# Performance work log

Measured on AMD Instinct MI355X. Metric: run time of the kernel, lower is better.

## Reference

```python
import jax, jax.numpy as jnp
import numpy as np

SEQ_LEN, BATCH, INPUT_SIZE, HIDDEN = 512, 64, 256, 512


def setup_inputs() -> dict:
    key = jax.random.key(0)
    k_x, k_wih, k_whh, k_bih, k_bhh = jax.random.split(key, 5)
    bound = 1.0 / np.sqrt(HIDDEN)  # torch nn.RNN init: U(-1/sqrt(H), 1/sqrt(H))
    x = jax.random.normal(k_x, (SEQ_LEN, BATCH, INPUT_SIZE), dtype=jnp.float32)
    h0 = jnp.zeros((1, BATCH, HIDDEN), dtype=jnp.float32)
    W_ih = jax.random.uniform(k_wih, (HIDDEN, INPUT_SIZE), minval=-bound, maxval=bound, dtype=jnp.float32)
    W_hh = jax.random.uniform(k_whh, (HIDDEN, HIDDEN), minval=-bound, maxval=bound, dtype=jnp.float32)
    b_ih = jax.random.uniform(k_bih, (HIDDEN,), minval=-bound, maxval=bound, dtype=jnp.float32)
    b_hh = jax.random.uniform(k_bhh, (HIDDEN,), minval=-bound, maxval=bound, dtype=jnp.float32)
    return {"x": x, "h0": h0, "W_ih": W_ih, "W_hh": W_hh, "b_ih": b_ih, "b_hh": b_hh}


def reference(x, h0, W_ih, W_hh, b_ih, b_hh):
    # Elman RNN: h_t = tanh(W_ih x_t + b_ih + W_hh h_{t-1} + b_hh)
    # Precompute the input projection for all timesteps (one big GEMM),
    # then scan the sequential recurrence.
    xW = jnp.einsum('tbi,hi->tbh', x, W_ih) + b_ih + b_hh  # (T, B, H)

    def step(h, xw_t):
        h_new = jnp.tanh(xw_t + h @ W_hh.T)  # (B, H)
        return h_new, h_new

    h_last, h_seq = jax.lax.scan(step, h0[0], xW)
    return h_seq, h_last[None]  # (T, B, H), (1, B, H)
```

## Files before the change

### kernel.cpp

```cpp
#include <hip/hip_runtime.h>


#define T_LEN 512
#define NBATCH 64
#define ISZ 256
#define HSZ 512

typedef __attribute__((ext_vector_type(8))) short short8;
typedef __attribute__((ext_vector_type(4))) int int4v;
typedef __attribute__((ext_vector_type(4))) float f32x4;

#define LOG2E2f 2.8853900817779268f
#define DEQ2C ((float)(2.8853900817779268 / (127.0 * 127.0 * 22.627416997969522)))

__device__ __forceinline__ unsigned short f2bf(float f) {
  unsigned u = __float_as_uint(f);
  u += 0x7fffu + ((u >> 16) & 1u);
  return (unsigned short)(u >> 16);
}
__device__ __forceinline__ float bf2f(unsigned short h) {
  return __uint_as_float(((unsigned)h) << 16);
}

__device__ __forceinline__ void split_bf(f32x4 a, f32x4 b, short8& hi, short8& lo) {
#pragma unroll
  for (int i = 0; i < 4; ++i) {
    unsigned short h = f2bf(a[i]);
    hi[i] = (short)h;
    lo[i] = (short)f2bf(a[i] - bf2f(h));
    unsigned short h2 = f2bf(b[i]);
    hi[i + 4] = (short)h2;
    lo[i + 4] = (short)f2bf(b[i] - bf2f(h2));
  }
}

__global__ __launch_bounds__(512) void xw_proj(
    const float* __restrict__ x, const float* __restrict__ Wih,
    const float* __restrict__ bih, const float* __restrict__ bhh,
    float* __restrict__ out) {
  __shared__ __align__(16) short xhi[16][264];
  __shared__ __align__(16) short xlo[16][264];

  const int tid = threadIdx.x;
  const int w  = tid >> 6;
  const int L  = tid & 63;
  const int lr = L & 15;
  const int lg = L >> 4;

  const int mhalf = blockIdx.x & 1;
  const int grp   = blockIdx.x >> 1;

  short8 Ahi[2][8], Alo[2][8];
  f32x4 bias[2];
  int mt[2];
#pragma unroll
  for (int m = 0; m < 2; ++m) {
    mt[m] = mhalf * 16 + 2 * w + m;
    int j = mt[m] * 16 + lr;
#pragma unroll
    for (int kt = 0; kt < 8; ++kt) {
      int k = kt * 32 + lg * 8;
      const f32x4 v0 = *(const f32x4*)(Wih + j * ISZ + k);
      const f32x4 v1 = *(const f32x4*)(Wih + j * ISZ + k + 4);
      split_bf(v0, v1, Ahi[m][kt], Alo[m][kt]);
    }
    int j0 = mt[m] * 16 + lg * 4;
    f32x4 b1 = *(const f32x4*)(bih + j0);
    f32x4 b2 = *(const f32x4*)(bhh + j0);
    bias[m] = (b1 + b2) * LOG2E2f;
  }

  for (int it = 0; it < 8; ++it) {
    const int tau = grp * 8 + it;
    const int t = tau >> 2;
    const int g = tau & 3;

    __syncthreads();
    {
      const int f   = tid * 8;
      const int row = f >> 8;
      const int i0  = f & 255;
      const float* p = x + ((size_t)(t * NBATCH + g * 16 + row) * ISZ + i0);
      const f32x4 v0 = *(const f32x4*)p;
      const f32x4 v1 = *(const f32x4*)(p + 4);
      short8 hi, lo;
      split_bf(v0, v1, hi, lo);
      *(short8*)(&xhi[row][i0]) = hi;
      *(short8*)(&xlo[row][i0]) = lo;
    }
    __syncthreads();

    f32x4 acc[2];
    acc[0] = f32x4{0.f, 0.f, 0.f, 0.f};
    acc[1] = f32x4{0.f, 0.f, 0.f, 0.f};
#pragma unroll
    for (int kt = 0; kt < 8; ++kt) {
      int koff = kt * 32 + lg * 8;
      short8 bh = *(const short8*)(&xhi[lr][koff]);
      short8 bl = *(const short8*)(&xlo[lr][koff]);
      acc[0] = __builtin_amdgcn_mfma_f32_16x16x32_bf16(Ahi[0][kt], bh, acc[0], 0, 0, 0);
      acc[1] = __builtin_amdgcn_mfma_f32_16x16x32_bf16(Ahi[1][kt], bh, acc[1], 0, 0, 0);
      acc[0] = __builtin_amdgcn_mfma_f32_16x16x32_bf16(Alo[0][kt], bh, acc[0], 0, 0, 0);
      acc[1] = __builtin_amdgcn_mfma_f32_16x16x32_bf16(Alo[1][kt], bh, acc[1], 0, 0, 0);
      acc[0] = __builtin_amdgcn_mfma_f32_16x16x32_bf16(Ahi[0][kt], bl, acc[0], 0, 0, 0);
      acc[1] = __builtin_amdgcn_mfma_f32_16x16x32_bf16(Ahi[1][kt], bl, acc[1], 0, 0, 0);
    }
#pragma unroll
    for (int m = 0; m < 2; ++m) {
      f32x4 r = acc[m] * LOG2E2f + bias[m];
      *(f32x4*)(out + (size_t)((((t * 4 + g) * 32 + mt[m]) * 64) + L) * 4) = r;
    }
  }
}

__global__ __launch_bounds__(512, 2) void rnn_scan_i8(
    const float* __restrict__ Whh, const float* __restrict__ h0,
    float* __restrict__ out) {
  __shared__ __align__(16) char hb[2 * 16 * 528];

  const int tid = threadIdx.x;
  const int w  = tid >> 6;
  const int L  = tid & 63;
  const int lr = L & 15;
  const int lg = L >> 4;
  const int g  = blockIdx.x;

  const float QS = 127.0f * 22.627416997969522f;

  int4v A[4][8];
#pragma unroll
  for (int m = 0; m < 4; ++m) {
    const int j = (4 * w + m) * 16 + lr;
#pragma unroll
    for (int kt = 0; kt < 8; ++kt) {
      const float* p = Whh + (size_t)j * HSZ + kt * 64 + lg * 16;
      int dw[4];
#pragma unroll
      for (int d = 0; d < 4; ++d) {
        f32x4 v = *(const f32x4*)(p + d * 4);
        int pk = 0;
#pragma unroll
        for (int i = 0; i < 4; ++i) {
          float q = __builtin_rintf(fminf(fmaxf(v[i] * QS, -127.f), 127.f));
          pk |= ((int)q & 255) << (8 * i);
        }
        dw[d] = pk;
      }
      A[m][kt] = int4v{dw[0], dw[1], dw[2], dw[3]};
    }
  }

  {
    const int row = tid >> 5;
    const int k0  = (tid & 31) * 16;
    const float* p = h0 + ((size_t)(g * 16 + row) * HSZ + k0);
    int dw[4];
#pragma unroll
    for (int c = 0; c < 4; ++c) {
      f32x4 v = *(const f32x4*)(p + c * 4);
      int pk = 0;
#pragma unroll
      for (int i = 0; i < 4; ++i) {
        float q = __builtin_rintf(fminf(fmaxf(v[i] * 127.f, -127.f), 127.f));
        pk |= ((int)q & 255) << (8 * i);
      }
      dw[c] = pk;
    }
    *(int4v*)(&hb[row * 528 + k0]) = int4v{dw[0], dw[1], dw[2], dw[3]};
  }
  __syncthreads();

  const int j0 = 4 * w * 16 + lg * 4;
  const char* xwp = (const char*)out + ((size_t)(g * 32 + 4 * w) * 64 + L) * 16;
  float* hsp = out + (size_t)(g * 16 + lr) * HSZ + j0;
  const int ldsr = lr * 528 + lg * 16;
  const int ldsw = lr * 528 + j0;

  f32x4 pend[4];
  f32x4 xwA[4], xwB[4];

#pragma unroll
  for (int m = 0; m < 4; ++m) xwA[m] = *(const f32x4*)(xwp + m * 1024);
  xwp += 131072;

#define RNN_STEP(XWC, XWN, P, DOSTORE) do {                                    \
    _Pragma("unroll")                                                          \
    for (int m = 0; m < 4; ++m) XWN[m] = *(const f32x4*)(xwp + m * 1024);      \
    xwp += 131072;                                                             \
    if (DOSTORE) {                                                             \
      _Pragma("unroll")                                                        \
      for (int m = 0; m < 4; ++m) *(f32x4*)(hsp + m * 16) = pend[m];           \
      hsp += NBATCH * HSZ;                                                     \
    }                                                                          \
    int4v B[8];                                                                \
    _Pragma("unroll")                                                          \
    for (int kt = 0; kt < 8; ++kt)                                             \
      B[kt] = *(const int4v*)(&hb[(P) * 8448 + ldsr + kt * 64]);               \
    int4v acc[4];                                                              \
    _Pragma("unroll")                                                          \
    for (int m = 0; m < 4; ++m) acc[m] = int4v{0, 0, 0, 0};                    \
    _Pragma("unroll")                                                          \
    for (int kt = 0; kt < 8; ++kt)                                             \
      _Pragma("unroll")                                                        \
      for (int m = 0; m < 4; ++m)                                              \
        acc[m] = __builtin_amdgcn_mfma_i32_16x16x64_i8(A[m][kt], B[kt],        \
                                                       acc[m], 0, 0, 0);       \
    _Pragma("unroll")                                                          \
    for (int m = 0; m < 4; ++m) {                                              \
      unsigned qi[4];                                                          \
      f32x4 hh;                                                                \
      _Pragma("unroll")                                                        \
      for (int r = 0; r < 4; ++r) {                                            \
        float y2 = fmaf((float)acc[m][r], DEQ2C, XWC[m][r]);                   \
        float e  = __builtin_amdgcn_exp2f(y2);                     \
        float rc = __builtin_amdgcn_rcpf(1.0f + e);                            \
        float hv = fmaf(-2.0f, rc, 1.0f);                         \
        hh[r] = hv;                                                            \
        qi[r] = __float_as_uint(fmaf(hv, 127.0f, 12582912.0f));                \
      }                                                                        \
      pend[m] = hh;                                                            \
      unsigned pp0 = __builtin_amdgcn_perm(qi[1], qi[0], 0x0c0c0400u);         \
      unsigned pp1 = __builtin_amdgcn_perm(qi[3], qi[2], 0x04000c0cu);         \
      *(unsigned*)(&hb[(1 - (P)) * 8448 + ldsw + m * 16]) = pp0 | pp1;         \
    }                                                                          \
    asm volatile("s_waitcnt lgkmcnt(0)\n\ts_barrier" ::: "memory");            \
  } while (0)

  RNN_STEP(xwA, xwB, 0, 0);
  for (int it = 0; it < 255; ++it) {
    RNN_STEP(xwB, xwA, 1, 1);
    RNN_STEP(xwA, xwB, 0, 1);
  }
  RNN_STEP(xwB, xwA, 1, 1);
#undef RNN_STEP

#pragma unroll
  for (int m = 0; m < 4; ++m) {
    *(f32x4*)(hsp + m * 16) = pend[m];
    *(f32x4*)(out + (size_t)T_LEN * NBATCH * HSZ +
              (size_t)(g * 16 + lr) * HSZ + j0 + m * 16) = pend[m];
  }
}

extern "C" void kernel_launch(void* const* d_in, const int* in_sizes, int n_in,
                              void* d_out, int out_size, void* d_ws, size_t ws_size,
                              hipStream_t stream) {
  const float* x   = (const float*)d_in[0];
  const float* h0  = (const float*)d_in[1];
  const float* Wih = (const float*)d_in[2];
  const float* Whh = (const float*)d_in[3];
  const float* bih = (const float*)d_in[4];
  const float* bhh = (const float*)d_in[5];
  float* out = (float*)d_out;

  xw_proj<<<512, 512, 0, stream>>>(x, Wih, bih, bhh, out);
  rnn_scan_i8<<<4, 512, 0, stream>>>(Whh, h0, out);
}
```

Before: 987.4 us.

## Interleave tanh epilogue of each row block with MFMAs of the next block

Restructures each recurrence step into a software pipeline. The MFMA chain for row block m+1 is interleaved with the exp/rcp/quantize epilogue of block m, and sched_group_barrier hints pair 2 MFMAs with 7 VALU ops. The aim is to hide the transcendental epilogue latency under matrix-core work on the critical serial path. The cost is a fixed schedule that may raise register pressure or disagree with the compiler's own ordering.

Measured after the change: 956.1 us. 1.03x faster.

```diff
diff --git a/kernel.cpp b/kernel.cpp
--- a/kernel.cpp
+++ b/kernel.cpp
@@ -12,6 +12,8 @@
 
 #define LOG2E2f 2.8853900817779268f
 #define DEQ2C ((float)(2.8853900817779268 / (127.0 * 127.0 * 22.627416997969522)))
+
+#define SGB __builtin_amdgcn_sched_group_barrier
 
 __device__ __forceinline__ unsigned short f2bf(float f) {
   unsigned u = __float_as_uint(f);
@@ -183,6 +185,34 @@
   for (int m = 0; m < 4; ++m) xwA[m] = *(const f32x4*)(xwp + m * 1024);
   xwp += 131072;
 
+#define EP_ELEM(XWC, E, R, QDST) do {                                          \
+    float y2_ = fmaf((float)acc[E][R], DEQ2C, XWC[E][R]);                      \
+    float ex_ = __builtin_amdgcn_exp2f(y2_);                       \
+    float rc_ = __builtin_amdgcn_rcpf(1.0f + ex_);                             \
+    float hv_ = fmaf(-2.0f, rc_, 1.0f);                           \
+    pend[E][R] = hv_;                                                          \
+    QDST = __float_as_uint(fmaf(hv_, 127.0f, 12582912.0f));                    \
+  } while (0)
+
+#define SLOT(XWC, M, E, KT, R, QDST) do {                                      \
+    acc[M] = __builtin_amdgcn_mfma_i32_16x16x64_i8(A[M][KT], B[KT], acc[M], 0, 0, 0);      \
+    acc[M] = __builtin_amdgcn_mfma_i32_16x16x64_i8(A[M][(KT)+1], B[(KT)+1], acc[M], 0, 0, 0); \
+    EP_ELEM(XWC, E, R, QDST);                                                  \
+    SGB(0x8, 2, 0);                                               \
+    SGB(0x2, 7, 0);                                          \
+  } while (0)
+
+#define PHASE(XWC, M, E, WB) do {                                              \
+    unsigned q0_, q1_, q2_, q3_;                                               \
+    SLOT(XWC, M, E, 0, 0, q0_);                                                \
+    SLOT(XWC, M, E, 2, 1, q1_);                                                \
+    SLOT(XWC, M, E, 4, 2, q2_);                                                \
+    SLOT(XWC, M, E, 6, 3, q3_);                                                \
+    unsigned pp0_ = __builtin_amdgcn_perm(q1_, q0_, 0x0c0c0400u);              \
+    unsigned pp1_ = __builtin_amdgcn_perm(q3_, q2_, 0x04000c0cu);              \
+    *(unsigned*)(&hb[(WB) + ldsw + (E) * 16]) = pp0_ | pp1_;                   \
+  } while (0)
+
 #define RNN_STEP(XWC, XWN, P, DOSTORE) do {                                    \
     _Pragma("unroll")                                                          \
     for (int m = 0; m < 4; ++m) XWN[m] = *(const f32x4*)(xwp + m * 1024);      \
@@ -199,29 +229,25 @@
     int4v acc[4];                                                              \
     _Pragma("unroll")                                                          \
     for (int m = 0; m < 4; ++m) acc[m] = int4v{0, 0, 0, 0};                    \
+    const int wb_ = (1 - (P)) * 8448;                                          \
+                    \
     _Pragma("unroll")                                                          \
     for (int kt = 0; kt < 8; ++kt)                                             \
-      _Pragma("unroll")                                                        \
-      for (int m = 0; m < 4; ++m)                                              \
-        acc[m] = __builtin_amdgcn_mfma_i32_16x16x64_i8(A[m][kt], B[kt],        \
-                                                       acc[m], 0, 0, 0);       \
-    _Pragma("unroll")                                                          \
-    for (int m = 0; m < 4; ++m) {                                              \
-      unsigned qi[4];                                                          \
-      f32x4 hh;                                                                \
-      _Pragma("unroll")                                                        \
-      for (int r = 0; r < 4; ++r) {                                            \
-        float y2 = fmaf((float)acc[m][r], DEQ2C, XWC[m][r]);                   \
-        float e  = __builtin_amdgcn_exp2f(y2);                     \
-        float rc = __builtin_amdgcn_rcpf(1.0f + e);                            \
-        float hv = fmaf(-2.0f, rc, 1.0f);                         \
-        hh[r] = hv;                                                            \
-        qi[r] = __float_as_uint(fmaf(hv, 127.0f, 12582912.0f));                \
-      }                                                                        \
-      pend[m] = hh;                                                            \
-      unsigned pp0 = __builtin_amdgcn_perm(qi[1], qi[0], 0x0c0c0400u);         \
-      unsigned pp1 = __builtin_amdgcn_perm(qi[3], qi[2], 0x04000c0cu);         \
-      *(unsigned*)(&hb[(1 - (P)) * 8448 + ldsw + m * 16]) = pp0 | pp1;         \
+      acc[0] = __builtin_amdgcn_mfma_i32_16x16x64_i8(A[0][kt], B[kt], acc[0], 0, 0, 0); \
+                                     \
+    PHASE(XWC, 1, 0, wb_);                                                     \
+    PHASE(XWC, 2, 1, wb_);                                                     \
+    PHASE(XWC, 3, 2, wb_);                                                     \
+                                                        \
+    {                                                                          \
+      unsigned q0_, q1_, q2_, q3_;                                             \
+      EP_ELEM(XWC, 3, 0, q0_);                                                 \
+      EP_ELEM(XWC, 3, 1, q1_);                                                 \
+      EP_ELEM(XWC, 3, 2, q2_);                                                 \
+      EP_ELEM(XWC, 3, 3, q3_);                                                 \
+      unsigned pp0_ = __builtin_amdgcn_perm(q1_, q0_, 0x0c0c0400u);            \
+      unsigned pp1_ = __builtin_amdgcn_perm(q3_, q2_, 0x04000c0cu);            \
+      *(unsigned*)(&hb[wb_ + ldsw + 3 * 16]) = pp0_ | pp1_;                    \
     }                                                                          \
     asm volatile("s_waitcnt lgkmcnt(0)\n\ts_barrier" ::: "memory");            \
   } while (0)
@@ -233,6 +259,9 @@
   }
   RNN_STEP(xwB, xwA, 1, 1);
 #undef RNN_STEP
+#undef PHASE
+#undef SLOT
+#undef EP_ELEM
 
 #pragma unroll
   for (int m = 0; m < 4; ++m) {
```
